# Kernel tuning notes

Measured on AMD Instinct MI355X. Metric: run time of the kernel, lower is better.

## Reference

```python
import jax, jax.numpy as jnp
import numpy as np
from jax import lax

S = 48          # fixed crop size (original crops are ragged; fixed here for batching)
EPS = 0.1       # Sinkhorn entropic regularization
ITERS = 50      # Sinkhorn iterations
TINY = 1e-8


def setup_inputs() -> dict:
    key = jax.random.key(0)
    k1, k2, k3 = jax.random.split(key, 3)
    B, C, H, W = 16, 5, 160, 160
    hm_gt = jax.random.uniform(k1, (B, C, H, W), dtype=jnp.float32)
    hm_pred = jax.random.uniform(k2, (B, C, H, W), dtype=jnp.float32)
    tops = jax.random.randint(k3, (B, 8, 2), 0, 112, dtype=jnp.int32)  # (y, x) per rect
    return {"hm_gt": hm_gt, "hm_pred": hm_pred, "tops": tops}


def _geometry_distance(s):
    # pairwise Euclidean distance between pixel centers of an s x s crop -> [s*s, s*s]
    ys, xs = jnp.meshgrid(jnp.arange(s, dtype=jnp.float32),
                          jnp.arange(s, dtype=jnp.float32), indexing="ij")
    pts = jnp.stack([ys.ravel(), xs.ravel()], axis=-1)          # [s*s, 2]
    d2 = jnp.sum((pts[:, None, :] - pts[None, :, :]) ** 2, -1)  # [s*s, s*s]
    return jnp.sqrt(d2)


def _crop_all(hm, tops):
    # hm: [B, C, H, W], tops: [B, R, 2] -> crops [B, R, C, S, S]
    def crop_one(hm_b, top):  # hm_b [C,H,W], top [2]
        return lax.dynamic_slice(hm_b, (0, top[0], top[1]), (hm_b.shape[0], S, S))
    return jax.vmap(lambda hb, tb: jax.vmap(lambda t: crop_one(hb, t))(tb))(hm, tops)


def reference(hm_gt, hm_pred, tops):
    B, C, H, W = hm_gt.shape
    n = S * S
    dist = _geometry_distance(S)            # [n, n]
    K = jnp.exp(-dist / EPS)                # Gibbs kernel
    M = K * dist                            # for the transport cost readout

    a = _crop_all(hm_gt, tops).reshape(-1, n)    # [N, n]
    b = _crop_all(hm_pred, tops).reshape(-1, n)  # [N, n]
    a = a / (jnp.sum(a, -1, keepdims=True) + TINY)   # normalize to marginals
    b = b / (jnp.sum(b, -1, keepdims=True) + TINY)

    N = a.shape[0]
    u0 = jnp.full((N, n), 1.0 / n, dtype=a.dtype)
    v0 = jnp.full((N, n), 1.0 / n, dtype=a.dtype)

    def body(carry, _):
        u, v = carry
        v = b / (u @ K + TINY)      # [N,n] @ [n,n]
        u = a / (v @ K.T + TINY)
        return (u, v), None

    (u, v), _ = lax.scan(body, (u0, v0), None, length=ITERS)
    # loss per crop: sum_ij u_i K_ij dist_ij v_j
    loss = jnp.sum((u @ M) * v)
    return loss
```

## Files before the change

### kernel.cpp

```cpp
#include <hip/hip_runtime.h>

#define TINYF 1e-8f
#define NITER 50

typedef __attribute__((ext_vector_type(2))) float v2f;

__device__ __forceinline__ float wWs(float v) {
    return __int_as_float(__builtin_amdgcn_update_dpp(0, __float_as_int(v), 0x138, 0xf, 0xf, true));
}
__device__ __forceinline__ float wEs(float v) {
    return __int_as_float(__builtin_amdgcn_update_dpp(0, __float_as_int(v), 0x130, 0xf, 0xf, true));
}
__device__ __forceinline__ v2f wW(v2f v) { v2f r; r.x = wWs(v.x); r.y = wWs(v.y); return r; }
__device__ __forceinline__ v2f wE(v2f v) { v2f r; r.x = wEs(v.x); r.y = wEs(v.y); return r; }
__device__ __forceinline__ v2f rcp2(v2f v) {
    v2f r; r.x = __builtin_amdgcn_rcpf(v.x); r.y = __builtin_amdgcn_rcpf(v.y); return r;
}
__device__ __forceinline__ v2f pfma(float k, v2f a, v2f c) {
    v2f kv; kv.x = k; kv.y = k;
    return __builtin_elementwise_fma(kv, a, c);
}

__global__ void __launch_bounds__(256)
sinkhorn_colpk(const float* __restrict__ hm_gt,
               const float* __restrict__ hm_pred,
               const int* __restrict__ tops,
               float* __restrict__ out) {
    __shared__ v2f ES[2][6][4][64];
    __shared__ float sred[2][4];

    const int t = threadIdx.x;
    const int W = t >> 6;
    const int l = t & 63;
    const bool act = (l < 48);

    {
        const int p = W >> 1, r = W & 1;
        ((float*)&ES[p][0][2 + r][l])[0] = 0.f;
        ((float*)&ES[p][5][r][l])[1] = 0.f;
    }

    const int blk = blockIdx.x;
    const int bi = blk / 40, rr = (blk / 5) % 8, cc = blk % 5;
    const int y0 = tops[(bi * 8 + rr) * 2 + 0];
    const int x0 = tops[(bi * 8 + rr) * 2 + 1];
    const float* srcA = hm_gt + (size_t)(bi * 5 + cc) * 25600;
    const float* srcB = hm_pred + (size_t)(bi * 5 + cc) * 25600;

    v2f va[6], vb[6];
    float sA = 0.f, sB = 0.f;
    const int rbx = y0 + 6 * W;
    const int rby = y0 + 24 + 6 * W;
#pragma unroll
    for (int r = 0; r < 6; ++r) {
        const int gx = (rbx + r) * 160 + x0 + l;
        const int gy = (rby + r) * 160 + x0 + l;
        va[r].x = act ? srcA[gx] : 0.f;
        va[r].y = act ? srcA[gy] : 0.f;
        vb[r].x = act ? srcB[gx] : 0.f;
        vb[r].y = act ? srcB[gy] : 0.f;
        sA += va[r].x + va[r].y;
        sB += vb[r].x + vb[r].y;
    }
#pragma unroll
    for (int o = 1; o < 64; o <<= 1) {
        sA += __shfl_xor(sA, o, 64);
        sB += __shfl_xor(sB, o, 64);
    }
    if (l == 0) { sred[0][W] = sA; sred[1][W] = sB; }
    __syncthreads();
    sA = sred[0][0] + sred[0][1] + sred[0][2] + sred[0][3];
    sB = sred[1][0] + sred[1][1] + sred[1][2] + sred[1][3];
    const float nA = 1.0f / (sA + TINYF);
    const float nB = 1.0f / (sB + TINYF);
#pragma unroll
    for (int r = 0; r < 6; ++r) {
        va[r].x *= nA; va[r].y *= nA;
        vb[r].x *= nB; vb[r].y *= nB;
    }

    const float e10 = expf(-1.0f / 0.1f);
    const float e2  = expf(-sqrtf(2.0f) / 0.1f);
    const float e20 = expf(-2.0f / 0.1f);

    v2f xu[6], xv[6], acc[6];
    const float u0 = 1.0f / 2304.0f;
#pragma unroll
    for (int r = 0; r < 6; ++r) { xu[r].x = act ? u0 : 0.f; xu[r].y = act ? u0 : 0.f; }

    auto publish = [&](const v2f (&y)[6], int p) {
        ES[p][W + 1][0][l] = y[0];
        ES[p][W + 1][1][l] = y[1];
        ES[p][W + 1][2][l] = y[4];
        ES[p][W + 1][3][l] = y[5];
        if (W == 3) {
            ((float*)&ES[p][0][2][l])[1] = y[4].x;
            ((float*)&ES[p][0][3][l])[1] = y[5].x;
        }
        if (W == 0) {
            ((float*)&ES[p][5][0][l])[0] = y[0].y;
            ((float*)&ES[p][5][1][l])[0] = y[1].y;
        }
        __syncthreads();
    };

    auto conv = [&](const v2f (&x)[6], int p, bool CENTER,
                    float K01, float K11, float K02) {
        const v2f um2 = ES[p][W][2][l];
        const v2f um1 = ES[p][W][3][l];
        const v2f up6 = ES[p][W + 2][0][l];
        const v2f up7 = ES[p][W + 2][1][l];
        v2f s1[8], s2[6];
#pragma unroll
        for (int r = 0; r < 6; ++r) {
            const v2f w1 = wW(x[r]), e1 = wE(x[r]);
            s1[r + 1] = w1 + e1;
            s2[r] = wW(w1) + wE(e1);
        }
        s1[0] = wW(um1) + wE(um1);
        s1[7] = wW(up6) + wE(up6);
#pragma unroll
        for (int r = 0; r < 6; ++r) {
            const v2f up1 = (r == 0) ? um1 : x[r - 1];
            const v2f dn1 = (r == 5) ? up6 : x[r + 1];
            const v2f up2 = (r == 0) ? um2 : ((r == 1) ? um1 : x[r - 2]);
            const v2f dn2 = (r == 4) ? up6 : ((r == 5) ? up7 : x[r + 2]);
            v2f a;
            if (CENTER) { a = x[r]; } else { a.x = 0.f; a.y = 0.f; }
            a = pfma(K01, s1[r + 1] + (up1 + dn1), a);
            a = pfma(K11, s1[r] + s1[r + 2], a);
            a = pfma(K02, s2[r] + (up2 + dn2), a);
            acc[r] = a;
        }
    };

    publish(xu, 0);

#pragma unroll 1
    for (int it = 0; it < NITER; ++it) {
        conv(xu, 0, true, e10, e2, e20);
#pragma unroll
        for (int r = 0; r < 6; ++r) {
            v2f d; d.x = acc[r].x + TINYF; d.y = acc[r].y + TINYF;
            xv[r] = vb[r] * rcp2(d);
        }
        publish(xv, 1);

        conv(xv, 1, true, e10, e2, e20);
#pragma unroll
        for (int r = 0; r < 6; ++r) {
            v2f d; d.x = acc[r].x + TINYF; d.y = acc[r].y + TINYF;
            xu[r] = va[r] * rcp2(d);
        }
        publish(xu, 0);
    }

    const float s2f = sqrtf(2.0f);
    const float m01 = e10, m02 = e20 * 2.0f, m11 = e2 * s2f;
    conv(xu, 0, false, m01, m11, m02);
    v2f ls; ls.x = 0.f; ls.y = 0.f;
#pragma unroll
    for (int r = 0; r < 6; ++r) ls += acc[r] * xv[r];
    float lsum = ls.x + ls.y;

#pragma unroll
    for (int o = 1; o < 64; o <<= 1) lsum += __shfl_xor(lsum, o, 64);
    if (l == 0) sred[0][W] = lsum;
    __syncthreads();
    if (t == 0)
        atomicAdd(out, sred[0][0] + sred[0][1] + sred[0][2] + sred[0][3]);
}

extern "C" void kernel_launch(void* const* d_in, const int* in_sizes, int n_in,
                              void* d_out, int out_size, void* d_ws, size_t ws_size,
                              hipStream_t stream) {
    (void)in_sizes; (void)n_in; (void)out_size; (void)d_ws; (void)ws_size;
    const float* hm_gt = (const float*)d_in[0];
    const float* hm_pred = (const float*)d_in[1];
    const int* tops = (const int*)d_in[2];
    float* out = (float*)d_out;

    hipMemsetAsync(out, 0, sizeof(float), stream);
    sinkhorn_colpk<<<dim3(640), dim3(256), 0, stream>>>(hm_gt, hm_pred, tops, out);
}
```

Baseline: 172.3 us.

## Reorder Sinkhorn half-step to overlap LDS halo loads with interior rows

The convolution and reciprocal update are fused into one half-step. Interior rows that need no halo are computed first, and each boundary row is written to shared memory as soon as it is ready. The DPP horizontal partial sums for the new iterate are computed right after it is produced (prep), moving that work off the critical path after the barrier. This is meant to hide LDS read latency and shorten the dependency chain between barriers, at the cost of more live registers for the cached s1/s2 arrays.

```diff
diff --git a/kernel.cpp b/kernel.cpp
--- a/kernel.cpp
+++ b/kernel.cpp
@@ -22,10 +22,10 @@
 }
 
 __global__ void __launch_bounds__(256)
-sinkhorn_colpk(const float* __restrict__ hm_gt,
-               const float* __restrict__ hm_pred,
-               const int* __restrict__ tops,
-               float* __restrict__ out) {
+sinkhorn_plq(const float* __restrict__ hm_gt,
+             const float* __restrict__ hm_pred,
+             const int* __restrict__ tops,
+             float* __restrict__ out) {
     __shared__ v2f ES[2][6][4][64];
     __shared__ float sred[2][4];
 
@@ -82,85 +82,139 @@
     const float e10 = expf(-1.0f / 0.1f);
     const float e2  = expf(-sqrtf(2.0f) / 0.1f);
     const float e20 = expf(-2.0f / 0.1f);
-
-    v2f xu[6], xv[6], acc[6];
+    const v2f tiny = {TINYF, TINYF};
+
+    v2f xu[6], xv[6];
     const float u0 = 1.0f / 2304.0f;
 #pragma unroll
     for (int r = 0; r < 6; ++r) { xu[r].x = act ? u0 : 0.f; xu[r].y = act ? u0 : 0.f; }
 
-    auto publish = [&](const v2f (&y)[6], int p) {
-        ES[p][W + 1][0][l] = y[0];
-        ES[p][W + 1][1][l] = y[1];
-        ES[p][W + 1][2][l] = y[4];
-        ES[p][W + 1][3][l] = y[5];
-        if (W == 3) {
-            ((float*)&ES[p][0][2][l])[1] = y[4].x;
-            ((float*)&ES[p][0][3][l])[1] = y[5].x;
-        }
-        if (W == 0) {
-            ((float*)&ES[p][5][0][l])[0] = y[0].y;
-            ((float*)&ES[p][5][1][l])[0] = y[1].y;
-        }
-        __syncthreads();
+    v2f s1o[6], s2o[6];
+    auto prep = [&](const v2f (&x)[6]) {
+#pragma unroll
+        for (int r = 0; r < 6; ++r) {
+            const v2f w1 = wW(x[r]), e1 = wE(x[r]);
+            s1o[r] = w1 + e1;
+            s2o[r] = wW(w1) + wE(e1);
+        }
     };
 
-    auto conv = [&](const v2f (&x)[6], int p, bool CENTER,
-                    float K01, float K11, float K02) {
-        const v2f um2 = ES[p][W][2][l];
+    auto half = [&](const v2f (&x)[6], v2f (&o)[6], const v2f (&co)[6],
+                    int p, int q) {
         const v2f um1 = ES[p][W][3][l];
         const v2f up6 = ES[p][W + 2][0][l];
+        const v2f um2 = ES[p][W][2][l];
         const v2f up7 = ES[p][W + 2][1][l];
-        v2f s1[8], s2[6];
-#pragma unroll
-        for (int r = 0; r < 6; ++r) {
-            const v2f w1 = wW(x[r]), e1 = wE(x[r]);
-            s1[r + 1] = w1 + e1;
-            s2[r] = wW(w1) + wE(e1);
-        }
-        s1[0] = wW(um1) + wE(um1);
-        s1[7] = wW(up6) + wE(up6);
-#pragma unroll
-        for (int r = 0; r < 6; ++r) {
-            const v2f up1 = (r == 0) ? um1 : x[r - 1];
-            const v2f dn1 = (r == 5) ? up6 : x[r + 1];
-            const v2f up2 = (r == 0) ? um2 : ((r == 1) ? um1 : x[r - 2]);
-            const v2f dn2 = (r == 4) ? up6 : ((r == 5) ? up7 : x[r + 2]);
-            v2f a;
-            if (CENTER) { a = x[r]; } else { a.x = 0.f; a.y = 0.f; }
-            a = pfma(K01, s1[r + 1] + (up1 + dn1), a);
-            a = pfma(K11, s1[r] + s1[r + 2], a);
-            a = pfma(K02, s2[r] + (up2 + dn2), a);
-            acc[r] = a;
-        }
+        v2f a;
+        a = x[2];
+        a = pfma(e10, s1o[2] + (x[1] + x[3]), a);
+        a = pfma(e2,  s1o[1] + s1o[3], a);
+        a = pfma(e20, s2o[2] + (x[0] + x[4]), a);
+        o[2] = co[2] * rcp2(a + tiny);
+        a = x[3];
+        a = pfma(e10, s1o[3] + (x[2] + x[4]), a);
+        a = pfma(e2,  s1o[2] + s1o[4], a);
+        a = pfma(e20, s2o[3] + (x[1] + x[5]), a);
+        o[3] = co[3] * rcp2(a + tiny);
+        a = x[1];
+        a = pfma(e10, s1o[1] + (x[0] + x[2]), a);
+        a = pfma(e2,  s1o[0] + s1o[2], a);
+        a = pfma(e20, s2o[1] + (um1 + x[3]), a);
+        o[1] = co[1] * rcp2(a + tiny);
+        ES[q][W + 1][1][l] = o[1];
+        a = x[4];
+        a = pfma(e10, s1o[4] + (x[3] + x[5]), a);
+        a = pfma(e2,  s1o[3] + s1o[5], a);
+        a = pfma(e20, s2o[4] + (x[2] + up6), a);
+        o[4] = co[4] * rcp2(a + tiny);
+        ES[q][W + 1][2][l] = o[4];
+        const v2f s1m = wW(um1) + wE(um1);
+        const v2f s1p = wW(up6) + wE(up6);
+        a = x[0];
+        a = pfma(e10, s1o[0] + (um1 + x[1]), a);
+        a = pfma(e2,  s1m + s1o[1], a);
+        a = pfma(e20, s2o[0] + (um2 + x[2]), a);
+        o[0] = co[0] * rcp2(a + tiny);
+        ES[q][W + 1][0][l] = o[0];
+        a = x[5];
+        a = pfma(e10, s1o[5] + (x[4] + up6), a);
+        a = pfma(e2,  s1o[4] + s1p, a);
+        a = pfma(e20, s2o[5] + (x[3] + up7), a);
+        o[5] = co[5] * rcp2(a + tiny);
+        ES[q][W + 1][3][l] = o[5];
+        if (W == 3) {
+            ((float*)&ES[q][0][2][l])[1] = o[4].x;
+            ((float*)&ES[q][0][3][l])[1] = o[5].x;
+        }
+        if (W == 0) {
+            ((float*)&ES[q][5][0][l])[0] = o[0].y;
+            ((float*)&ES[q][5][1][l])[0] = o[1].y;
+        }
+        prep(o);
     };
 
-    publish(xu, 0);
+    {
+        ES[0][W + 1][0][l] = xu[0];
+        ES[0][W + 1][1][l] = xu[1];
+        ES[0][W + 1][2][l] = xu[4];
+        ES[0][W + 1][3][l] = xu[5];
+        if (W == 3) {
+            ((float*)&ES[0][0][2][l])[1] = xu[4].x;
+            ((float*)&ES[0][0][3][l])[1] = xu[5].x;
+        }
+        if (W == 0) {
+            ((float*)&ES[0][5][0][l])[0] = xu[0].y;
+            ((float*)&ES[0][5][1][l])[0] = xu[1].y;
+        }
+        prep(xu);
+        __syncthreads();
+    }
 
 #pragma unroll 1
     for (int it = 0; it < NITER; ++it) {
-        conv(xu, 0, true, e10, e2, e20);
-#pragma unroll
-        for (int r = 0; r < 6; ++r) {
-            v2f d; d.x = acc[r].x + TINYF; d.y = acc[r].y + TINYF;
-            xv[r] = vb[r] * rcp2(d);
-        }
-        publish(xv, 1);
-
-        conv(xv, 1, true, e10, e2, e20);
-#pragma unroll
-        for (int r = 0; r < 6; ++r) {
-            v2f d; d.x = acc[r].x + TINYF; d.y = acc[r].y + TINYF;
-            xu[r] = va[r] * rcp2(d);
-        }
-        publish(xu, 0);
+        half(xu, xv, vb, 0, 1);
+        __syncthreads();
+        half(xv, xu, va, 1, 0);
+        __syncthreads();
     }
 
     const float s2f = sqrtf(2.0f);
     const float m01 = e10, m02 = e20 * 2.0f, m11 = e2 * s2f;
-    conv(xu, 0, false, m01, m11, m02);
-    v2f ls; ls.x = 0.f; ls.y = 0.f;
-#pragma unroll
-    for (int r = 0; r < 6; ++r) ls += acc[r] * xv[r];
+    v2f ls = {0.f, 0.f};
+    {
+        const v2f um1 = ES[0][W][3][l];
+        const v2f up6 = ES[0][W + 2][0][l];
+        const v2f um2 = ES[0][W][2][l];
+        const v2f up7 = ES[0][W + 2][1][l];
+        const v2f s1m = wW(um1) + wE(um1);
+        const v2f s1p = wW(up6) + wE(up6);
+        const v2f zero = {0.f, 0.f};
+        v2f a;
+        a = pfma(m01, s1o[0] + (um1 + xu[1]), zero);
+        a = pfma(m11, s1m + s1o[1], a);
+        a = pfma(m02, s2o[0] + (um2 + xu[2]), a);
+        ls += a * xv[0];
+        a = pfma(m01, s1o[1] + (xu[0] + xu[2]), zero);
+        a = pfma(m11, s1o[0] + s1o[2], a);
+        a = pfma(m02, s2o[1] + (um1 + xu[3]), a);
+        ls += a * xv[1];
+        a = pfma(m01, s1o[2] + (xu[1] + xu[3]), zero);
+        a = pfma(m11, s1o[1] + s1o[3], a);
+        a = pfma(m02, s2o[2] + (xu[0] + xu[4]), a);
+        ls += a * xv[2];
+        a = pfma(m01, s1o[3] + (xu[2] + xu[4]), zero);
+        a = pfma(m11, s1o[2] + s1o[4], a);
+        a = pfma(m02, s2o[3] + (xu[1] + xu[5]), a);
+        ls += a * xv[3];
+        a = pfma(m01, s1o[4] + (xu[3] + xu[5]), zero);
+        a = pfma(m11, s1o[3] + s1o[5], a);
+        a = pfma(m02, s2o[4] + (xu[2] + up6), a);
+        ls += a * xv[4];
+        a = pfma(m01, s1o[5] + (xu[4] + up6), zero);
+        a = pfma(m11, s1o[4] + s1p, a);
+        a = pfma(m02, s2o[5] + (xu[3] + up7), a);
+        ls += a * xv[5];
+    }
     float lsum = ls.x + ls.y;
 
 #pragma unroll
@@ -181,5 +235,5 @@
     float* out = (float*)d_out;
 
     hipMemsetAsync(out, 0, sizeof(float), stream);
-    sinkhorn_colpk<<<dim3(640), dim3(256), 0, stream>>>(hm_gt, hm_pred, tops, out);
-}
+    sinkhorn_plq<<<dim3(640), dim3(256), 0, stream>>>(hm_gt, hm_pred, tops, out);
+}
```

Result: faster. 166.9 us (-3.1%).

## Use ghost-row halos to fuse both half-steps with one barrier per iteration

Applied to the files above, without the earlier changes.

Each wave now exchanges a 4-row halo of u instead of 2 rows. It redundantly computes v over 10 rows (its own 6 plus 2 ghost rows on each side), so the u update needs no second shared-memory exchange. This halves the number of __syncthreads and LDS publishes per Sinkhorn iteration. In exchange it adds redundant stencil work on the ghost rows, more LDS traffic per publish, and more registers for the extended b and v arrays.

```diff
diff --git a/kernel.cpp b/kernel.cpp
--- a/kernel.cpp
+++ b/kernel.cpp
@@ -22,11 +22,11 @@
 }
 
 __global__ void __launch_bounds__(256)
-sinkhorn_colpk(const float* __restrict__ hm_gt,
+sinkhorn_ghost(const float* __restrict__ hm_gt,
                const float* __restrict__ hm_pred,
                const int* __restrict__ tops,
                float* __restrict__ out) {
-    __shared__ v2f ES[2][6][4][64];
+    __shared__ v2f ES[2][6][8][64];
     __shared__ float sred[2][4];
 
     const int t = threadIdx.x;
@@ -35,9 +35,12 @@
     const bool act = (l < 48);
 
     {
-        const int p = W >> 1, r = W & 1;
-        ((float*)&ES[p][0][2 + r][l])[0] = 0.f;
-        ((float*)&ES[p][5][r][l])[1] = 0.f;
+        const int p = W >> 1;
+        const int j0 = (W & 1) * 2;
+        ((float*)&ES[p][0][4 + j0][l])[0] = 0.f;
+        ((float*)&ES[p][0][5 + j0][l])[0] = 0.f;
+        ((float*)&ES[p][5][j0][l])[1] = 0.f;
+        ((float*)&ES[p][5][j0 + 1][l])[1] = 0.f;
     }
 
     const int blk = blockIdx.x;
@@ -47,20 +50,27 @@
     const float* srcA = hm_gt + (size_t)(bi * 5 + cc) * 25600;
     const float* srcB = hm_pred + (size_t)(bi * 5 + cc) * 25600;
 
-    v2f va[6], vb[6];
+    v2f va[6], be[10];
     float sA = 0.f, sB = 0.f;
-    const int rbx = y0 + 6 * W;
-    const int rby = y0 + 24 + 6 * W;
 #pragma unroll
     for (int r = 0; r < 6; ++r) {
-        const int gx = (rbx + r) * 160 + x0 + l;
-        const int gy = (rby + r) * 160 + x0 + l;
+        const int gx = (y0 + 6 * W + r) * 160 + x0 + l;
+        const int gy = (y0 + 24 + 6 * W + r) * 160 + x0 + l;
         va[r].x = act ? srcA[gx] : 0.f;
         va[r].y = act ? srcA[gy] : 0.f;
-        vb[r].x = act ? srcB[gx] : 0.f;
-        vb[r].y = act ? srcB[gy] : 0.f;
         sA += va[r].x + va[r].y;
-        sB += vb[r].x + vb[r].y;
+    }
+#pragma unroll
+    for (int i = 0; i < 10; ++i) {
+        const int cx = 6 * W + i - 2;
+        const int cy = 24 + 6 * W + i - 2;
+        const bool vx = (cx >= 0);
+        const bool vy = (cy < 48);
+        const int gx = (y0 + (vx ? cx : 0)) * 160 + x0 + l;
+        const int gy = (y0 + (vy ? cy : 47)) * 160 + x0 + l;
+        be[i].x = (act && vx) ? srcB[gx] : 0.f;
+        be[i].y = (act && vy) ? srcB[gy] : 0.f;
+        if (i >= 2 && i < 8) { sB += be[i].x + be[i].y; }
     }
 #pragma unroll
     for (int o = 1; o < 64; o <<= 1) {
@@ -74,93 +84,128 @@
     const float nA = 1.0f / (sA + TINYF);
     const float nB = 1.0f / (sB + TINYF);
 #pragma unroll
-    for (int r = 0; r < 6; ++r) {
-        va[r].x *= nA; va[r].y *= nA;
-        vb[r].x *= nB; vb[r].y *= nB;
-    }
+    for (int r = 0; r < 6; ++r) { va[r].x *= nA; va[r].y *= nA; }
+#pragma unroll
+    for (int i = 0; i < 10; ++i) { be[i].x *= nB; be[i].y *= nB; }
 
     const float e10 = expf(-1.0f / 0.1f);
     const float e2  = expf(-sqrtf(2.0f) / 0.1f);
     const float e20 = expf(-2.0f / 0.1f);
-
-    v2f xu[6], xv[6], acc[6];
+    const v2f tiny = {TINYF, TINYF};
+
+    v2f xu[6], vt[10];
     const float u0 = 1.0f / 2304.0f;
 #pragma unroll
     for (int r = 0; r < 6; ++r) { xu[r].x = act ? u0 : 0.f; xu[r].y = act ? u0 : 0.f; }
 
-    auto publish = [&](const v2f (&y)[6], int p) {
-        ES[p][W + 1][0][l] = y[0];
-        ES[p][W + 1][1][l] = y[1];
-        ES[p][W + 1][2][l] = y[4];
-        ES[p][W + 1][3][l] = y[5];
+    auto publish = [&](int q) {
+        ES[q][W + 1][0][l] = xu[0];
+        ES[q][W + 1][1][l] = xu[1];
+        ES[q][W + 1][2][l] = xu[2];
+        ES[q][W + 1][3][l] = xu[3];
+        ES[q][W + 1][4][l] = xu[2];
+        ES[q][W + 1][5][l] = xu[3];
+        ES[q][W + 1][6][l] = xu[4];
+        ES[q][W + 1][7][l] = xu[5];
         if (W == 3) {
-            ((float*)&ES[p][0][2][l])[1] = y[4].x;
-            ((float*)&ES[p][0][3][l])[1] = y[5].x;
+            ((float*)&ES[q][0][4][l])[1] = xu[2].x;
+            ((float*)&ES[q][0][5][l])[1] = xu[3].x;
+            ((float*)&ES[q][0][6][l])[1] = xu[4].x;
+            ((float*)&ES[q][0][7][l])[1] = xu[5].x;
         }
         if (W == 0) {
-            ((float*)&ES[p][5][0][l])[0] = y[0].y;
-            ((float*)&ES[p][5][1][l])[0] = y[1].y;
-        }
-        __syncthreads();
+            ((float*)&ES[q][5][0][l])[0] = xu[0].y;
+            ((float*)&ES[q][5][1][l])[0] = xu[1].y;
+            ((float*)&ES[q][5][2][l])[0] = xu[2].y;
+            ((float*)&ES[q][5][3][l])[0] = xu[3].y;
+        }
     };
 
-    auto conv = [&](const v2f (&x)[6], int p, bool CENTER,
-                    float K01, float K11, float K02) {
-        const v2f um2 = ES[p][W][2][l];
-        const v2f um1 = ES[p][W][3][l];
-        const v2f up6 = ES[p][W + 2][0][l];
-        const v2f up7 = ES[p][W + 2][1][l];
-        v2f s1[8], s2[6];
-#pragma unroll
-        for (int r = 0; r < 6; ++r) {
-            const v2f w1 = wW(x[r]), e1 = wE(x[r]);
-            s1[r + 1] = w1 + e1;
-            s2[r] = wW(w1) + wE(e1);
-        }
-        s1[0] = wW(um1) + wE(um1);
-        s1[7] = wW(up6) + wE(up6);
-#pragma unroll
-        for (int r = 0; r < 6; ++r) {
-            const v2f up1 = (r == 0) ? um1 : x[r - 1];
-            const v2f dn1 = (r == 5) ? up6 : x[r + 1];
-            const v2f up2 = (r == 0) ? um2 : ((r == 1) ? um1 : x[r - 2]);
-            const v2f dn2 = (r == 4) ? up6 : ((r == 5) ? up7 : x[r + 2]);
-            v2f a;
-            if (CENTER) { a = x[r]; } else { a.x = 0.f; a.y = 0.f; }
-            a = pfma(K01, s1[r + 1] + (up1 + dn1), a);
-            a = pfma(K11, s1[r] + s1[r + 2], a);
-            a = pfma(K02, s2[r] + (up2 + dn2), a);
-            acc[r] = a;
-        }
-    };
-
-    publish(xu, 0);
+    publish(0);
+    __syncthreads();
 
 #pragma unroll 1
     for (int it = 0; it < NITER; ++it) {
-        conv(xu, 0, true, e10, e2, e20);
-#pragma unroll
-        for (int r = 0; r < 6; ++r) {
-            v2f d; d.x = acc[r].x + TINYF; d.y = acc[r].y + TINYF;
-            xv[r] = vb[r] * rcp2(d);
-        }
-        publish(xv, 1);
-
-        conv(xv, 1, true, e10, e2, e20);
-#pragma unroll
-        for (int r = 0; r < 6; ++r) {
-            v2f d; d.x = acc[r].x + TINYF; d.y = acc[r].y + TINYF;
-            xu[r] = va[r] * rcp2(d);
-        }
-        publish(xu, 0);
+        const int p = it & 1;
+        v2f hu[4], hd[4];
+#pragma unroll
+        for (int j = 0; j < 4; ++j) {
+            hu[j] = ES[p][W][4 + j][l];
+            hd[j] = ES[p][W + 2][j][l];
+        }
+        auto uat = [&](int r) -> v2f {
+            return (r < 0) ? hu[r + 4] : ((r < 6) ? xu[r] : hd[r - 6]);
+        };
+        {
+            v2f w1a = wW(uat(-3)), e1a = wE(uat(-3));
+            v2f s1a = w1a + e1a;
+            v2f w1c = wW(uat(-2)), e1c = wE(uat(-2));
+            v2f s1b = w1c + e1c;
+#pragma unroll
+            for (int i = 0; i < 10; ++i) {
+                const int r = i - 2;
+                v2f w1n = wW(uat(r + 1)), e1n = wE(uat(r + 1));
+                v2f s1n = w1n + e1n;
+                v2f s2c = wW(w1c) + wE(e1c);
+                v2f a = uat(r);
+                a = pfma(e10, s1b + (uat(r - 1) + uat(r + 1)), a);
+                a = pfma(e2,  s1a + s1n, a);
+                a = pfma(e20, s2c + (uat(r - 2) + uat(r + 2)), a);
+                vt[i] = be[i] * rcp2(a + tiny);
+                s1a = s1b; s1b = s1n; w1c = w1n; e1c = e1n;
+            }
+        }
+        {
+            v2f w1a = wW(vt[1]), e1a = wE(vt[1]);
+            v2f s1a = w1a + e1a;
+            v2f w1c = wW(vt[2]), e1c = wE(vt[2]);
+            v2f s1b = w1c + e1c;
+#pragma unroll
+            for (int r = 0; r < 6; ++r) {
+                v2f w1n = wW(vt[r + 3]), e1n = wE(vt[r + 3]);
+                v2f s1n = w1n + e1n;
+                v2f s2c = wW(w1c) + wE(e1c);
+                v2f a = vt[r + 2];
+                a = pfma(e10, s1b + (vt[r + 1] + vt[r + 3]), a);
+                a = pfma(e2,  s1a + s1n, a);
+                a = pfma(e20, s2c + (vt[r] + vt[r + 4]), a);
+                xu[r] = va[r] * rcp2(a + tiny);
+                s1a = s1b; s1b = s1n; w1c = w1n; e1c = e1n;
+            }
+        }
+        publish(p ^ 1);
+        __syncthreads();
     }
 
     const float s2f = sqrtf(2.0f);
     const float m01 = e10, m02 = e20 * 2.0f, m11 = e2 * s2f;
-    conv(xu, 0, false, m01, m11, m02);
-    v2f ls; ls.x = 0.f; ls.y = 0.f;
-#pragma unroll
-    for (int r = 0; r < 6; ++r) ls += acc[r] * xv[r];
+    v2f ls = {0.f, 0.f};
+    {
+        const v2f um2 = ES[0][W][6][l];
+        const v2f um1 = ES[0][W][7][l];
+        const v2f hp6 = ES[0][W + 2][0][l];
+        const v2f hp7 = ES[0][W + 2][1][l];
+        auto uat = [&](int r) -> v2f {
+            return (r == -2) ? um2 : (r == -1) ? um1 :
+                   (r == 6) ? hp6 : (r == 7) ? hp7 : xu[(r < 0) ? 0 : ((r > 5) ? 5 : r)];
+        };
+        v2f w1a = wW(um1), e1a = wE(um1);
+        v2f s1a = w1a + e1a;
+        v2f w1c = wW(xu[0]), e1c = wE(xu[0]);
+        v2f s1b = w1c + e1c;
+        const v2f zero = {0.f, 0.f};
+#pragma unroll
+        for (int r = 0; r < 6; ++r) {
+            v2f w1n = wW(uat(r + 1)), e1n = wE(uat(r + 1));
+            v2f s1n = w1n + e1n;
+            v2f s2c = wW(w1c) + wE(e1c);
+            v2f a = pfma(m01, s1b + (uat(r - 1) + uat(r + 1)), zero);
+            a = pfma(m11, s1a + s1n, a);
+            a = pfma(m02, s2c + (uat(r - 2) + uat(r + 2)), a);
+            ls += a * vt[r + 2];
+            s1a = s1b; s1b = s1n; w1c = w1n; e1c = e1n;
+        }
+    }
     float lsum = ls.x + ls.y;
 
 #pragma unroll
@@ -181,5 +226,5 @@
     float* out = (float*)d_out;
 
     hipMemsetAsync(out, 0, sizeof(float), stream);
-    sinkhorn_colpk<<<dim3(640), dim3(256), 0, stream>>>(hm_gt, hm_pred, tops, out);
-}
+    sinkhorn_ghost<<<dim3(640), dim3(256), 0, stream>>>(hm_gt, hm_pred, tops, out);
+}
```

Result: slower. 188.1 us (+9.1%).
